# Kernel optimization log

Measured on AMD Instinct MI355X. Metric: run time of the kernel, lower is better.

## Reference

```python
import jax, jax.numpy as jnp
import numpy as np

B, I, H, M, A, R, S, O = 256, 512, 1024, 128, 2048, 4, 3, 512
RS = R * M                      # read_size = num_heads * memory_content_size
P_READ = M + S + 3              # key + shift + (beta, gate, gamma) per read head
P = R * P_READ + (3 * M + S + 3)  # write head adds erase(M) + add(M)


def setup_inputs() -> dict:
    key = jax.random.key(0)
    ks = jax.random.split(key, 16)
    x = jax.random.normal(ks[0], (B, I), dtype=jnp.float32)
    h_prev = 0.1 * jax.random.normal(ks[1], (B, H), dtype=jnp.float32)
    c_prev = 0.1 * jax.random.normal(ks[2], (B, H), dtype=jnp.float32)
    read_w_prev = jax.nn.softmax(jax.random.normal(ks[3], (B, R, A)), axis=-1)
    write_w_prev = jax.nn.softmax(jax.random.normal(ks[4], (B, A)), axis=-1)
    # init_state uses normal(mean=0.5, std=0.2) for memory
    memory_prev = 0.5 + 0.2 * jax.random.normal(ks[5], (B, M, A), dtype=jnp.float32)
    read_vec_prev = 0.1 * jax.random.normal(ks[6], (B, RS), dtype=jnp.float32)
    sc = 0.02
    Wx = sc * jax.random.normal(ks[7], (I + RS, 4 * H), dtype=jnp.float32)
    Wh = sc * jax.random.normal(ks[8], (H, 4 * H), dtype=jnp.float32)
    b_lstm = jnp.zeros((4 * H,), dtype=jnp.float32)
    Wo_h = sc * jax.random.normal(ks[9], (H, O), dtype=jnp.float32)
    bo_h = jnp.zeros((O,), dtype=jnp.float32)
    Wint = sc * jax.random.normal(ks[10], (H, P), dtype=jnp.float32)
    b_int = jnp.zeros((P,), dtype=jnp.float32)
    Wout = sc * jax.random.normal(ks[11], (RS, O), dtype=jnp.float32)
    b_out = jnp.zeros((O,), dtype=jnp.float32)
    return dict(x=x, h_prev=h_prev, c_prev=c_prev, read_w_prev=read_w_prev,
                write_w_prev=write_w_prev, memory_prev=memory_prev,
                read_vec_prev=read_vec_prev, Wx=Wx, Wh=Wh, b_lstm=b_lstm,
                Wo_h=Wo_h, bo_h=bo_h, Wint=Wint, b_int=b_int, Wout=Wout, b_out=b_out)


def _address(k, beta, g, s, gamma, w_prev, mem):
    """NTM/DNC addressing: cosine content sim -> softmax -> gate -> circular shift -> sharpen.
    k: [B,Rh,M], beta/g/gamma: [B,Rh], s: [B,Rh,S], w_prev: [B,Rh,A], mem: [B,M,A] -> w: [B,Rh,A]"""
    eps = 1e-8
    kn = jnp.linalg.norm(k, axis=-1, keepdims=True)          # [B,Rh,1]
    mn = jnp.linalg.norm(mem, axis=1)                        # [B,A]
    sim = jnp.einsum('brm,bma->bra', k, mem) / (kn * mn[:, None, :] + eps)
    w_c = jax.nn.softmax(beta[..., None] * sim, axis=-1)
    w_g = g[..., None] * w_c + (1.0 - g[..., None]) * w_prev
    # circular convolution over S shift offsets centered at 0
    rolled = jnp.stack([jnp.roll(w_g, off, axis=-1) for off in range(-(S // 2), S // 2 + 1)], axis=-1)  # [B,Rh,A,S]
    w_s = jnp.einsum('bras,brs->bra', rolled, s)
    w_pow = (w_s + 1e-12) ** gamma[..., None]
    return w_pow / (jnp.sum(w_pow, axis=-1, keepdims=True) + eps)


def reference(x, h_prev, c_prev, read_w_prev, write_w_prev, memory_prev, read_vec_prev,
              Wx, Wh, b_lstm, Wo_h, bo_h, Wint, b_int, Wout, b_out):
    b = x.shape[0]
    # ---- controller (LSTM over [input, prev read vector]) ----
    z = jnp.concatenate([x, read_vec_prev], axis=-1) @ Wx + h_prev @ Wh + b_lstm
    i_g, f_g, g_g, o_g = jnp.split(z, 4, axis=-1)
    c = jax.nn.sigmoid(f_g) * c_prev + jax.nn.sigmoid(i_g) * jnp.tanh(g_g)
    h = jax.nn.sigmoid(o_g) * jnp.tanh(c)
    output_from_hidden = h @ Wo_h + bo_h
    p = h @ Wint + b_int                                    # interface update_data
    # ---- read heads ----
    pr = p[:, :R * P_READ].reshape(b, R, P_READ)
    k_r = pr[..., :M]
    beta_r = jax.nn.softplus(pr[..., M])
    g_r = jax.nn.sigmoid(pr[..., M + 1])
    gamma_r = 1.0 + jax.nn.softplus(pr[..., M + 2])
    s_r = jax.nn.softmax(pr[..., M + 3:], axis=-1)
    w_read = _address(k_r, beta_r, g_r, s_r, gamma_r, read_w_prev, memory_prev)
    # ---- write head ----
    pw = p[:, R * P_READ:]
    k_w = pw[:, :M]
    beta_w = jax.nn.softplus(pw[:, M])
    g_w = jax.nn.sigmoid(pw[:, M + 1])
    gamma_w = 1.0 + jax.nn.softplus(pw[:, M + 2])
    s_w = jax.nn.softmax(pw[:, M + 3:M + 3 + S], axis=-1)
    erase = jax.nn.sigmoid(pw[:, M + 3 + S:2 * M + 3 + S])
    add = pw[:, 2 * M + 3 + S:]
    w_write = _address(k_w[:, None], beta_w[:, None], g_w[:, None], s_w[:, None],
                       gamma_w[:, None], write_w_prev[:, None], memory_prev)[:, 0]
    # ---- read from PREVIOUS memory (as in DNCCell.forward) ----
    read_vec = jnp.einsum('bma,bra->brm', memory_prev, w_read).reshape(b, RS)
    # ---- erase/add memory edit ----
    memory_new = memory_prev * (1.0 - jnp.einsum('bm,ba->bma', erase, w_write)) \
               + jnp.einsum('bm,ba->bma', add, w_write)
    final_output = output_from_hidden + read_vec @ Wout + b_out
    return final_output, memory_new
```

## Files before the change

### kernel.cpp

```cpp
#include <hip/hip_runtime.h>
#include <math.h>

#define B_ 256
#define I_ 512
#define H_ 1024
#define M_ 128
#define A_ 2048
#define R_ 4
#define S_ 3
#define O_ 512
#define RS_ 512
#define P_ 926
#define PW_OFF 536

typedef unsigned short ushort_t;
typedef __attribute__((ext_vector_type(8))) short bf16x8;
typedef __attribute__((ext_vector_type(4))) float f32x4;

__device__ __forceinline__ float sigmoidf_(float x) { return 1.0f / (1.0f + expf(-x)); }
__device__ __forceinline__ float softplusf_(float x) {
    return (x > 20.0f) ? x : log1pf(expf(x));
}
__device__ __forceinline__ ushort_t f2bf(float f) {
    unsigned int u = __float_as_uint(f);
    u = (u + 0x7FFFu + ((u >> 16) & 1u)) >> 16;
    return (ushort_t)u;
}

__device__ __forceinline__ float block_sum_(float v, float* red) {
    #pragma unroll
    for (int off = 32; off; off >>= 1) v += __shfl_down(v, off, 64);
    __syncthreads();
    if ((threadIdx.x & 63) == 0) red[threadIdx.x >> 6] = v;
    __syncthreads();
    return red[0] + red[1] + red[2] + red[3];
}
__device__ __forceinline__ float block_max_(float v, float* red) {
    #pragma unroll
    for (int off = 32; off; off >>= 1) v = fmaxf(v, __shfl_down(v, off, 64));
    __syncthreads();
    if ((threadIdx.x & 63) == 0) red[threadIdx.x >> 6] = v;
    __syncthreads();
    return fmaxf(fmaxf(red[0], red[1]), fmaxf(red[2], red[3]));
}

__global__ __launch_bounds__(256) void prep_kernel(
    const float* __restrict__ x, const float* __restrict__ rv,
    const float* __restrict__ hp, ushort_t* __restrict__ xin)
{
    int idx = blockIdx.x * 256 + threadIdx.x;
    int b = idx >> 11, j = idx & 2047;
    float v;
    if (j < 512)       v = x[b * 512 + j];
    else if (j < 1024) v = rv[b * 512 + (j - 512)];
    else               v = hp[b * 1024 + (j - 1024)];
    xin[idx] = f2bf(v);
}

__global__ __launch_bounds__(256) void transpose_bf16_k(
    const float* __restrict__ W, ushort_t* __restrict__ WT,
    int K, int N, int ostride, int koff)
{
    __shared__ float tile[32][33];
    int k0 = blockIdx.y * 32, n0 = blockIdx.x * 32;
    int tx = threadIdx.x & 31, ty = threadIdx.x >> 5;
    #pragma unroll
    for (int i = 0; i < 4; ++i) {
        int k = ty + i * 8;
        int n = n0 + tx;
        float v = (n < N) ? W[(size_t)(k0 + k) * N + n] : 0.0f;
        tile[tx][k] = v;
    }
    __syncthreads();
    #pragma unroll
    for (int i = 0; i < 4; ++i) {
        int nl = ty + i * 8;
        int n = n0 + nl;
        if (n < N) WT[(size_t)n * ostride + koff + k0 + tx] = f2bf(tile[nl][tx]);
    }
}

template<bool NALIGN>
__global__ __launch_bounds__(256) void gemm_bf16_k(
    const ushort_t* __restrict__ A, int lda,
    const ushort_t* __restrict__ BT, int ldb,
    const float* __restrict__ bias,
    const float* __restrict__ Cin,
    float* __restrict__ C,
    int N, int K)
{
    __shared__ ushort_t As[64][40];
    __shared__ ushort_t Bs[64][40];
    int tid = threadIdx.x;
    int bm0 = blockIdx.y * 64, bn0 = blockIdx.x * 64;
    int srow = tid >> 2;
    int scol = (tid & 3) << 3;
    int wv = tid >> 6, l = tid & 63;
    int wm = (wv & 1) * 32, wn = (wv >> 1) * 32;
    int lane16 = l & 15, quad = l >> 4;

    f32x4 z4 = {0.0f, 0.0f, 0.0f, 0.0f};
    f32x4 acc00 = z4, acc01 = z4, acc10 = z4, acc11 = z4;

    const ushort_t* ap = A + (size_t)(bm0 + srow) * lda + scol;
    bool bvalid = NALIGN || (bn0 + srow) < N;
    const ushort_t* bp = BT + (size_t)(bn0 + srow) * ldb + scol;
    float4 fz = {0.0f, 0.0f, 0.0f, 0.0f};

    for (int k0 = 0; k0 < K; k0 += 32) {
        *(float4*)&As[srow][scol] = *(const float4*)(ap + k0);
        if (bvalid) *(float4*)&Bs[srow][scol] = *(const float4*)(bp + k0);
        else        *(float4*)&Bs[srow][scol] = fz;
        __syncthreads();
        bf16x8 a0 = *(const bf16x8*)&As[wm + lane16][quad * 8];
        bf16x8 a1 = *(const bf16x8*)&As[wm + 16 + lane16][quad * 8];
        bf16x8 b0 = *(const bf16x8*)&Bs[wn + lane16][quad * 8];
        bf16x8 b1 = *(const bf16x8*)&Bs[wn + 16 + lane16][quad * 8];
        acc00 = __builtin_amdgcn_mfma_f32_16x16x32_bf16(a0, b0, acc00, 0, 0, 0);
        acc01 = __builtin_amdgcn_mfma_f32_16x16x32_bf16(a0, b1, acc01, 0, 0, 0);
        acc10 = __builtin_amdgcn_mfma_f32_16x16x32_bf16(a1, b0, acc10, 0, 0, 0);
        acc11 = __builtin_amdgcn_mfma_f32_16x16x32_bf16(a1, b1, acc11, 0, 0, 0);
        __syncthreads();
    }

    #pragma unroll
    for (int gi = 0; gi < 2; ++gi) {
        #pragma unroll
        for (int gj = 0; gj < 2; ++gj) {
            const f32x4& acc = gi == 0 ? (gj == 0 ? acc00 : acc01)
                                       : (gj == 0 ? acc10 : acc11);
            int col = bn0 + wn + gj * 16 + lane16;
            if (NALIGN || col < N) {
                float badd = bias ? bias[col] : 0.0f;
                #pragma unroll
                for (int r2 = 0; r2 < 4; ++r2) {
                    int row = bm0 + wm + gi * 16 + quad * 4 + r2;
                    float v = acc[r2] + badd;
                    if (Cin) v += Cin[(size_t)row * N + col];
                    C[(size_t)row * N + col] = v;
                }
            }
        }
    }
}

__global__ __launch_bounds__(256) void gates_kernel(
    const float* __restrict__ z, const float* __restrict__ c_prev,
    ushort_t* __restrict__ h)
{
    int idx = blockIdx.x * 256 + threadIdx.x;
    int b = idx >> 10, j = idx & 1023;
    const float* zb = z + (size_t)b * 4096;
    float zi = zb[j], zf = zb[1024 + j], zg = zb[2048 + j], zo = zb[3072 + j];
    float c = sigmoidf_(zf) * c_prev[idx] + sigmoidf_(zi) * tanhf(zg);
    h[idx] = f2bf(sigmoidf_(zo) * tanhf(c));
}

__global__ __launch_bounds__(256) void sim_kernel(
    const float* __restrict__ mem, const float* __restrict__ p,
    float* __restrict__ dots,
    float* __restrict__ mn)
{
    int b = blockIdx.y;
    int a = blockIdx.x * 256 + threadIdx.x;
    __shared__ float ks[5][M_];
    for (int idx = threadIdx.x; idx < 5 * M_; idx += 256) {
        int h = idx >> 7, m = idx & 127;
        ks[h][m] = p[(size_t)b * P_ + (h < 4 ? h * 134 + m : PW_OFF + m)];
    }
    __syncthreads();
    const float* mb = mem + (size_t)b * M_ * A_ + a;
    float d0 = 0, d1 = 0, d2 = 0, d3 = 0, d4 = 0, nn = 0;
    #pragma unroll 8
    for (int m = 0; m < M_; ++m) {
        float v = mb[(size_t)m * A_];
        d0 += v * ks[0][m]; d1 += v * ks[1][m]; d2 += v * ks[2][m];
        d3 += v * ks[3][m]; d4 += v * ks[4][m];
        nn += v * v;
    }
    size_t base = (size_t)b * 5 * A_ + a;
    dots[base + 0 * A_] = d0; dots[base + 1 * A_] = d1; dots[base + 2 * A_] = d2;
    dots[base + 3 * A_] = d3; dots[base + 4 * A_] = d4;
    mn[(size_t)b * A_ + a] = sqrtf(nn);
}

__global__ __launch_bounds__(256) void address_kernel(
    const float* __restrict__ p, const float* __restrict__ dots,
    const float* __restrict__ mn,
    const float* __restrict__ read_w_prev, const float* __restrict__ write_w_prev,
    float* __restrict__ w_read, float* __restrict__ w_write)
{
    int head = blockIdx.x;
    int b = blockIdx.y;
    int t = threadIdx.x;
    __shared__ float wg[A_];
    __shared__ float red[4];

    const float* pp = p + (size_t)b * P_ + (head < 4 ? head * 134 : PW_OFF);
    float beta  = softplusf_(pp[128]);
    float g     = sigmoidf_(pp[129]);
    float gamma = 1.0f + softplusf_(pp[130]);
    float e0 = pp[131], e1 = pp[132], e2 = pp[133];
    float smax = fmaxf(e0, fmaxf(e1, e2));
    float x0 = expf(e0 - smax), x1 = expf(e1 - smax), x2 = expf(e2 - smax);
    float sden = x0 + x1 + x2;
    float s0 = x0 / sden, s1 = x1 / sden, s2 = x2 / sden;

    float kacc = 0.0f;
    if (t < M_) { float kv = pp[t]; kacc = kv * kv; }
    float kn = sqrtf(block_sum_(kacc, red));

    const float* db = dots + ((size_t)b * 5 + head) * A_;
    const float* mb = mn + (size_t)b * A_;
    float logit[8];
    float lmax = -1e30f;
    #pragma unroll
    for (int i = 0; i < 8; ++i) {
        int a = t + 256 * i;
        float sim = db[a] / (kn * mb[a] + 1e-8f);
        logit[i] = beta * sim;
        lmax = fmaxf(lmax, logit[i]);
    }
    lmax = block_max_(lmax, red);
    float ex[8]; float lsum = 0.0f;
    #pragma unroll
    for (int i = 0; i < 8; ++i) { ex[i] = expf(logit[i] - lmax); lsum += ex[i]; }
    lsum = block_sum_(lsum, red);
    float inv_lsum = 1.0f / lsum;

    const float* wprev = (head < 4) ? read_w_prev + ((size_t)b * 4 + head) * A_
                                    : write_w_prev + (size_t)b * A_;
    #pragma unroll
    for (int i = 0; i < 8; ++i) {
        int a = t + 256 * i;
        wg[a] = g * (ex[i] * inv_lsum) + (1.0f - g) * wprev[a];
    }
    __syncthreads();
    float wpow[8]; float psum = 0.0f;
    #pragma unroll
    for (int i = 0; i < 8; ++i) {
        int a = t + 256 * i;
        float ws = s0 * wg[(a + 1) & (A_ - 1)] + s1 * wg[a] + s2 * wg[(a + A_ - 1) & (A_ - 1)];
        float wp2 = powf(ws + 1e-12f, gamma);
        wpow[i] = wp2; psum += wp2;
    }
    psum = block_sum_(psum, red);
    float inv = 1.0f / (psum + 1e-8f);
    float* wout = (head < 4) ? w_read + ((size_t)b * 4 + head) * A_
                             : w_write + (size_t)b * A_;
    #pragma unroll
    for (int i = 0; i < 8; ++i) wout[t + 256 * i] = wpow[i] * inv;
}

__global__ __launch_bounds__(256) void update_kernel(
    const float* __restrict__ mem, const float* __restrict__ p,
    const float* __restrict__ w_read, const float* __restrict__ w_write,
    float* __restrict__ mem_new,
    ushort_t* __restrict__ read_vec)
{
    int bm = blockIdx.x;
    int b = bm >> 7, m = bm & 127;
    int t = threadIdx.x;
    int wv = t >> 6, l = t & 63;
    const float* pw = p + (size_t)b * P_ + PW_OFF;
    float er = sigmoidf_(pw[134 + m]);
    float ad = pw[262 + m];
    const float* mrow = mem + ((size_t)b * M_ + m) * A_;
    const float* wwb  = w_write + (size_t)b * A_;
    const float* wr   = w_read + (size_t)b * 4 * A_;
    float* orow = mem_new + ((size_t)b * M_ + m) * A_;
    float s[4] = {0, 0, 0, 0};
    int abase = wv * 512 + l;
    #pragma unroll
    for (int i = 0; i < 8; ++i) {
        int a = abase + 64 * i;
        float v = mrow[a];
        float ww = wwb[a];
        orow[a] = v * (1.0f - er * ww) + ad * ww;
        s[0] += v * wr[a];
        s[1] += v * wr[A_ + a];
        s[2] += v * wr[2 * A_ + a];
        s[3] += v * wr[3 * A_ + a];
    }
    __shared__ float part[4][4];
    #pragma unroll
    for (int r = 0; r < 4; ++r) {
        float v = s[r];
        #pragma unroll
        for (int off = 32; off; off >>= 1) v += __shfl_down(v, off, 64);
        if (l == 0) part[wv][r] = v;
    }
    __syncthreads();
    if (t < 4) {
        float sum = part[0][t] + part[1][t] + part[2][t] + part[3][t];
        read_vec[(size_t)b * RS_ + t * M_ + m] = f2bf(sum);
    }
}

extern "C" void kernel_launch(void* const* d_in, const int* in_sizes, int n_in,
                              void* d_out, int out_size, void* d_ws, size_t ws_size,
                              hipStream_t stream) {
    const float* x            = (const float*)d_in[0];
    const float* h_prev       = (const float*)d_in[1];
    const float* c_prev       = (const float*)d_in[2];
    const float* read_w_prev  = (const float*)d_in[3];
    const float* write_w_prev = (const float*)d_in[4];
    const float* memory_prev  = (const float*)d_in[5];
    const float* read_vec_prev= (const float*)d_in[6];
    const float* Wx           = (const float*)d_in[7];
    const float* Wh           = (const float*)d_in[8];
    const float* b_lstm       = (const float*)d_in[9];
    const float* Wo_h         = (const float*)d_in[10];
    const float* bo_h         = (const float*)d_in[11];
    const float* Wint         = (const float*)d_in[12];
    const float* b_int        = (const float*)d_in[13];
    const float* Wout         = (const float*)d_in[14];
    const float* b_out        = (const float*)d_in[15];
    float* out = (float*)d_out;
    float* mem_new_out = out + (size_t)B_ * O_;

    char* wsp = (char*)d_ws;
    ushort_t* xin_bf = (ushort_t*)wsp; wsp += (size_t)B_ * 2048 * 2;
    float* z         = (float*)wsp;    wsp += (size_t)B_ * 4096 * 4;
    ushort_t* h_bf   = (ushort_t*)wsp; wsp += (size_t)B_ * H_ * 2;
    float* p         = (float*)wsp;    wsp += (size_t)B_ * P_ * 4;
    float* out_h     = (float*)wsp;    wsp += (size_t)B_ * O_ * 4;
    float* dots      = (float*)wsp;    wsp += (size_t)B_ * 5 * A_ * 4;
    float* mn        = (float*)wsp;    wsp += (size_t)B_ * A_ * 4;
    float* w_read    = (float*)wsp;    wsp += (size_t)B_ * R_ * A_ * 4;
    float* w_write   = (float*)wsp;    wsp += (size_t)B_ * A_ * 4;
    ushort_t* rv_bf  = (ushort_t*)wsp; wsp += (size_t)B_ * RS_ * 2;
    ushort_t* WxhT   = (ushort_t*)wsp; wsp += (size_t)4096 * 2048 * 2;
    ushort_t* WoT    = (ushort_t*)wsp; wsp += (size_t)512 * 1024 * 2;
    ushort_t* WintT  = (ushort_t*)wsp; wsp += (size_t)926 * 1024 * 2;
    ushort_t* WoutT  = (ushort_t*)wsp; wsp += (size_t)512 * 512 * 2;

    transpose_bf16_k<<<dim3(4096 / 32, 1024 / 32), 256, 0, stream>>>(Wx,   WxhT,  1024, 4096, 2048, 0);
    transpose_bf16_k<<<dim3(4096 / 32, 1024 / 32), 256, 0, stream>>>(Wh,   WxhT,  1024, 4096, 2048, 1024);
    transpose_bf16_k<<<dim3(512 / 32, 1024 / 32),  256, 0, stream>>>(Wo_h, WoT,   1024, 512,  1024, 0);
    transpose_bf16_k<<<dim3(29, 1024 / 32),        256, 0, stream>>>(Wint, WintT, 1024, 926,  1024, 0);
    transpose_bf16_k<<<dim3(512 / 32, 512 / 32),   256, 0, stream>>>(Wout, WoutT, 512,  512,  512,  0);

    prep_kernel<<<dim3(B_ * 2048 / 256), 256, 0, stream>>>(x, read_vec_prev, h_prev, xin_bf);
    gemm_bf16_k<true><<<dim3(4096 / 64, B_ / 64), 256, 0, stream>>>(
        xin_bf, 2048, WxhT, 2048, b_lstm, nullptr, z, 4096, 2048);
    gates_kernel<<<dim3(B_ * H_ / 256), 256, 0, stream>>>(z, c_prev, h_bf);
    gemm_bf16_k<false><<<dim3(15, B_ / 64), 256, 0, stream>>>(
        h_bf, 1024, WintT, 1024, b_int, nullptr, p, P_, 1024);
    gemm_bf16_k<true><<<dim3(O_ / 64, B_ / 64), 256, 0, stream>>>(
        h_bf, 1024, WoT, 1024, bo_h, nullptr, out_h, O_, 1024);
    sim_kernel<<<dim3(A_ / 256, B_), 256, 0, stream>>>(memory_prev, p, dots, mn);
    address_kernel<<<dim3(5, B_), 256, 0, stream>>>(
        p, dots, mn, read_w_prev, write_w_prev, w_read, w_write);
    update_kernel<<<dim3(B_ * M_), 256, 0, stream>>>(
        memory_prev, p, w_read, w_write, mem_new_out, rv_bf);
    gemm_bf16_k<true><<<dim3(O_ / 64, B_ / 64), 256, 0, stream>>>(
        rv_bf, 512, WoutT, 512, b_out, out_h, out, O_, 512);
}
```

Before: 735.4 us.

## Split-K GEMMs, merge setup kernels, concatenate projection weights, vectorize elementwise kernels

Merges the five weight-transpose launches and the input-prep launch into one setup kernel. The LSTM GEMM and the combined interface+output projection GEMM now use a 4-way split-K so small-batch GEMMs fill more CUs, and the partial sums are reduced by their consumers (gates, sim, address, update, final GEMM). The gates and update kernels use vector loads, and the address kernel switches to fast exp/log intrinsics. In exchange it writes and reads more partial-sum traffic, and every consumer re-reduces the interface partials, with slightly lower precision in the exp/pow math.

```diff
diff --git a/kernel.cpp b/kernel.cpp
--- a/kernel.cpp
+++ b/kernel.cpp
@@ -12,10 +12,13 @@
 #define RS_ 512
 #define P_ 926
 #define PW_OFF 536
+#define NP_ 1438
+#define SK_ 4
 
 typedef unsigned short ushort_t;
 typedef __attribute__((ext_vector_type(8))) short bf16x8;
 typedef __attribute__((ext_vector_type(4))) float f32x4;
+typedef __attribute__((ext_vector_type(4))) unsigned short u16x4;
 
 __device__ __forceinline__ float sigmoidf_(float x) { return 1.0f / (1.0f + expf(-x)); }
 __device__ __forceinline__ float softplusf_(float x) {
@@ -27,6 +30,14 @@
     return (ushort_t)u;
 }
 
+__device__ __forceinline__ float pval(const float* __restrict__ pp,
+                                      const float* __restrict__ b_int,
+                                      int b, int col) {
+    size_t o = (size_t)b * NP_ + col;
+    size_t st = (size_t)B_ * NP_;
+    return b_int[col] + pp[o] + pp[o + st] + pp[o + 2 * st] + pp[o + 3 * st];
+}
+
 __device__ __forceinline__ float block_sum_(float v, float* red) {
     #pragma unroll
     for (int off = 32; off; off >>= 1) v += __shfl_down(v, off, 64);
@@ -44,11 +55,50 @@
     return fmaxf(fmaxf(red[0], red[1]), fmaxf(red[2], red[3]));
 }
 
-__global__ __launch_bounds__(256) void prep_kernel(
+__device__ __forceinline__ void transpose_tile(
+    const float* __restrict__ W, ushort_t* __restrict__ WT,
+    int K, int N, int ostride, int koff, int bx, int by, float (*tile)[33])
+{
+    int k0 = by * 32, n0 = bx * 32;
+    int tx = threadIdx.x & 31, ty = threadIdx.x >> 5;
+    #pragma unroll
+    for (int i = 0; i < 4; ++i) {
+        int k = ty + i * 8;
+        int n = n0 + tx;
+        float v = (n < N) ? W[(size_t)(k0 + k) * N + n] : 0.0f;
+        tile[tx][k] = v;
+    }
+    __syncthreads();
+    #pragma unroll
+    for (int i = 0; i < 4; ++i) {
+        int nl = ty + i * 8;
+        int n = n0 + nl;
+        if (n < N) WT[(size_t)n * ostride + koff + k0 + tx] = f2bf(tile[nl][tx]);
+    }
+}
+
+__global__ __launch_bounds__(256) void setup_kernel(
     const float* __restrict__ x, const float* __restrict__ rv,
-    const float* __restrict__ hp, ushort_t* __restrict__ xin)
-{
-    int idx = blockIdx.x * 256 + threadIdx.x;
+    const float* __restrict__ hp,
+    const float* __restrict__ Wx, const float* __restrict__ Wh,
+    const float* __restrict__ Wint, const float* __restrict__ Wo_h,
+    const float* __restrict__ Wout,
+    ushort_t* __restrict__ xin, ushort_t* __restrict__ WxhT,
+    ushort_t* __restrict__ WpT, ushort_t* __restrict__ WoutT)
+{
+    __shared__ float tile[32][33];
+    int r = blockIdx.x;
+    if (r < 4096) { transpose_tile(Wx, WxhT, 1024, 4096, 2048, 0,    r % 128, r / 128, tile); return; }
+    r -= 4096;
+    if (r < 4096) { transpose_tile(Wh, WxhT, 1024, 4096, 2048, 1024, r % 128, r / 128, tile); return; }
+    r -= 4096;
+    if (r < 928)  { transpose_tile(Wint, WpT, 1024, 926, 1024, 0,    r % 29,  r / 29,  tile); return; }
+    r -= 928;
+    if (r < 512)  { transpose_tile(Wo_h, WpT + (size_t)926 * 1024, 1024, 512, 1024, 0, r % 16, r / 16, tile); return; }
+    r -= 512;
+    if (r < 256)  { transpose_tile(Wout, WoutT, 512, 512, 512, 0,    r % 16,  r / 16,  tile); return; }
+    r -= 256;
+    int idx = r * 256 + threadIdx.x;
     int b = idx >> 11, j = idx & 2047;
     float v;
     if (j < 512)       v = x[b * 512 + j];
@@ -57,42 +107,18 @@
     xin[idx] = f2bf(v);
 }
 
-__global__ __launch_bounds__(256) void transpose_bf16_k(
-    const float* __restrict__ W, ushort_t* __restrict__ WT,
-    int K, int N, int ostride, int koff)
-{
-    __shared__ float tile[32][33];
-    int k0 = blockIdx.y * 32, n0 = blockIdx.x * 32;
-    int tx = threadIdx.x & 31, ty = threadIdx.x >> 5;
-    #pragma unroll
-    for (int i = 0; i < 4; ++i) {
-        int k = ty + i * 8;
-        int n = n0 + tx;
-        float v = (n < N) ? W[(size_t)(k0 + k) * N + n] : 0.0f;
-        tile[tx][k] = v;
-    }
-    __syncthreads();
-    #pragma unroll
-    for (int i = 0; i < 4; ++i) {
-        int nl = ty + i * 8;
-        int n = n0 + nl;
-        if (n < N) WT[(size_t)n * ostride + koff + k0 + tx] = f2bf(tile[nl][tx]);
-    }
-}
-
 template<bool NALIGN>
 __global__ __launch_bounds__(256) void gemm_bf16_k(
     const ushort_t* __restrict__ A, int lda,
     const ushort_t* __restrict__ BT, int ldb,
-    const float* __restrict__ bias,
-    const float* __restrict__ Cin,
-    float* __restrict__ C,
-    int N, int K)
+    float* __restrict__ Cpart,
+    int N, int Ks)
 {
     __shared__ ushort_t As[64][40];
     __shared__ ushort_t Bs[64][40];
     int tid = threadIdx.x;
     int bm0 = blockIdx.y * 64, bn0 = blockIdx.x * 64;
+    int kbeg = blockIdx.z * Ks, kend = kbeg + Ks;
     int srow = tid >> 2;
     int scol = (tid & 3) << 3;
     int wv = tid >> 6, l = tid & 63;
@@ -107,7 +133,7 @@
     const ushort_t* bp = BT + (size_t)(bn0 + srow) * ldb + scol;
     float4 fz = {0.0f, 0.0f, 0.0f, 0.0f};
 
-    for (int k0 = 0; k0 < K; k0 += 32) {
+    for (int k0 = kbeg; k0 < kend; k0 += 32) {
         *(float4*)&As[srow][scol] = *(const float4*)(ap + k0);
         if (bvalid) *(float4*)&Bs[srow][scol] = *(const float4*)(bp + k0);
         else        *(float4*)&Bs[srow][scol] = fz;
@@ -123,6 +149,7 @@
         __syncthreads();
     }
 
+    float* C = Cpart + (size_t)blockIdx.z * gridDim.y * 64 * N;
     #pragma unroll
     for (int gi = 0; gi < 2; ++gi) {
         #pragma unroll
@@ -131,13 +158,10 @@
                                        : (gj == 0 ? acc10 : acc11);
             int col = bn0 + wn + gj * 16 + lane16;
             if (NALIGN || col < N) {
-                float badd = bias ? bias[col] : 0.0f;
                 #pragma unroll
                 for (int r2 = 0; r2 < 4; ++r2) {
                     int row = bm0 + wm + gi * 16 + quad * 4 + r2;
-                    float v = acc[r2] + badd;
-                    if (Cin) v += Cin[(size_t)row * N + col];
-                    C[(size_t)row * N + col] = v;
+                    C[(size_t)row * N + col] = acc[r2];
                 }
             }
         }
@@ -145,19 +169,37 @@
 }
 
 __global__ __launch_bounds__(256) void gates_kernel(
-    const float* __restrict__ z, const float* __restrict__ c_prev,
-    ushort_t* __restrict__ h)
-{
-    int idx = blockIdx.x * 256 + threadIdx.x;
-    int b = idx >> 10, j = idx & 1023;
-    const float* zb = z + (size_t)b * 4096;
-    float zi = zb[j], zf = zb[1024 + j], zg = zb[2048 + j], zo = zb[3072 + j];
-    float c = sigmoidf_(zf) * c_prev[idx] + sigmoidf_(zi) * tanhf(zg);
-    h[idx] = f2bf(sigmoidf_(zo) * tanhf(c));
+    const float* __restrict__ zpart, const float* __restrict__ b_lstm,
+    const float* __restrict__ c_prev, ushort_t* __restrict__ h)
+{
+    int g = blockIdx.x * 256 + threadIdx.x;
+    int b = g >> 8, j = (g & 255) << 2;
+    size_t st = (size_t)B_ * 4096;
+    size_t zb = (size_t)b * 4096 + j;
+    f32x4 zs[4];
+    #pragma unroll
+    for (int q = 0; q < 4; ++q) {
+        size_t o = zb + q * 1024;
+        f32x4 v = *(const f32x4*)(zpart + o);
+        v += *(const f32x4*)(zpart + o + st);
+        v += *(const f32x4*)(zpart + o + 2 * st);
+        v += *(const f32x4*)(zpart + o + 3 * st);
+        v += *(const f32x4*)(b_lstm + q * 1024 + j);
+        zs[q] = v;
+    }
+    f32x4 cp = *(const f32x4*)(c_prev + (size_t)b * 1024 + j);
+    u16x4 hv;
+    #pragma unroll
+    for (int e = 0; e < 4; ++e) {
+        float c = sigmoidf_(zs[1][e]) * cp[e] + sigmoidf_(zs[0][e]) * tanhf(zs[2][e]);
+        hv[e] = f2bf(sigmoidf_(zs[3][e]) * tanhf(c));
+    }
+    *(u16x4*)(h + (size_t)b * 1024 + j) = hv;
 }
 
 __global__ __launch_bounds__(256) void sim_kernel(
-    const float* __restrict__ mem, const float* __restrict__ p,
+    const float* __restrict__ mem, const float* __restrict__ pohpart,
+    const float* __restrict__ b_int,
     float* __restrict__ dots,
     float* __restrict__ mn)
 {
@@ -166,7 +208,8 @@
     __shared__ float ks[5][M_];
     for (int idx = threadIdx.x; idx < 5 * M_; idx += 256) {
         int h = idx >> 7, m = idx & 127;
-        ks[h][m] = p[(size_t)b * P_ + (h < 4 ? h * 134 + m : PW_OFF + m)];
+        int col = (h < 4) ? h * 134 + m : PW_OFF + m;
+        ks[h][m] = pval(pohpart, b_int, b, col);
     }
     __syncthreads();
     const float* mb = mem + (size_t)b * M_ * A_ + a;
@@ -185,8 +228,8 @@
 }
 
 __global__ __launch_bounds__(256) void address_kernel(
-    const float* __restrict__ p, const float* __restrict__ dots,
-    const float* __restrict__ mn,
+    const float* __restrict__ pohpart, const float* __restrict__ b_int,
+    const float* __restrict__ dots, const float* __restrict__ mn,
     const float* __restrict__ read_w_prev, const float* __restrict__ write_w_prev,
     float* __restrict__ w_read, float* __restrict__ w_write)
 {
@@ -196,18 +239,20 @@
     __shared__ float wg[A_];
     __shared__ float red[4];
 
-    const float* pp = p + (size_t)b * P_ + (head < 4 ? head * 134 : PW_OFF);
-    float beta  = softplusf_(pp[128]);
-    float g     = sigmoidf_(pp[129]);
-    float gamma = 1.0f + softplusf_(pp[130]);
-    float e0 = pp[131], e1 = pp[132], e2 = pp[133];
+    int pb = (head < 4) ? head * 134 : PW_OFF;
+    float beta  = softplusf_(pval(pohpart, b_int, b, pb + 128));
+    float g     = sigmoidf_(pval(pohpart, b_int, b, pb + 129));
+    float gamma = 1.0f + softplusf_(pval(pohpart, b_int, b, pb + 130));
+    float e0 = pval(pohpart, b_int, b, pb + 131);
+    float e1 = pval(pohpart, b_int, b, pb + 132);
+    float e2 = pval(pohpart, b_int, b, pb + 133);
     float smax = fmaxf(e0, fmaxf(e1, e2));
-    float x0 = expf(e0 - smax), x1 = expf(e1 - smax), x2 = expf(e2 - smax);
+    float x0 = __expf(e0 - smax), x1 = __expf(e1 - smax), x2 = __expf(e2 - smax);
     float sden = x0 + x1 + x2;
     float s0 = x0 / sden, s1 = x1 / sden, s2 = x2 / sden;
 
     float kacc = 0.0f;
-    if (t < M_) { float kv = pp[t]; kacc = kv * kv; }
+    if (t < M_) { float kv = pval(pohpart, b_int, b, pb + t); kacc = kv * kv; }
     float kn = sqrtf(block_sum_(kacc, red));
 
     const float* db = dots + ((size_t)b * 5 + head) * A_;
@@ -224,7 +269,7 @@
     lmax = block_max_(lmax, red);
     float ex[8]; float lsum = 0.0f;
     #pragma unroll
-    for (int i = 0; i < 8; ++i) { ex[i] = expf(logit[i] - lmax); lsum += ex[i]; }
+    for (int i = 0; i < 8; ++i) { ex[i] = __expf(logit[i] - lmax); lsum += ex[i]; }
     lsum = block_sum_(lsum, red);
     float inv_lsum = 1.0f / lsum;
 
@@ -241,7 +286,7 @@
     for (int i = 0; i < 8; ++i) {
         int a = t + 256 * i;
         float ws = s0 * wg[(a + 1) & (A_ - 1)] + s1 * wg[a] + s2 * wg[(a + A_ - 1) & (A_ - 1)];
-        float wp2 = powf(ws + 1e-12f, gamma);
+        float wp2 = __expf(gamma * __logf(ws + 1e-12f));
         wpow[i] = wp2; psum += wp2;
     }
     psum = block_sum_(psum, red);
@@ -253,7 +298,8 @@
 }
 
 __global__ __launch_bounds__(256) void update_kernel(
-    const float* __restrict__ mem, const float* __restrict__ p,
+    const float* __restrict__ mem, const float* __restrict__ pohpart,
+    const float* __restrict__ b_int,
     const float* __restrict__ w_read, const float* __restrict__ w_write,
     float* __restrict__ mem_new,
     ushort_t* __restrict__ read_vec)
@@ -262,25 +308,28 @@
     int b = bm >> 7, m = bm & 127;
     int t = threadIdx.x;
     int wv = t >> 6, l = t & 63;
-    const float* pw = p + (size_t)b * P_ + PW_OFF;
-    float er = sigmoidf_(pw[134 + m]);
-    float ad = pw[262 + m];
-    const float* mrow = mem + ((size_t)b * M_ + m) * A_;
-    const float* wwb  = w_write + (size_t)b * A_;
-    const float* wr   = w_read + (size_t)b * 4 * A_;
-    float* orow = mem_new + ((size_t)b * M_ + m) * A_;
+    float er = sigmoidf_(pval(pohpart, b_int, b, 670 + m));
+    float ad = pval(pohpart, b_int, b, 798 + m);
+    const f32x4* m4  = (const f32x4*)(mem + ((size_t)b * M_ + m) * A_);
+    const f32x4* ww4 = (const f32x4*)(w_write + (size_t)b * A_);
+    const f32x4* wr4 = (const f32x4*)(w_read + (size_t)b * 4 * A_);
+    f32x4* o4 = (f32x4*)(mem_new + ((size_t)b * M_ + m) * A_);
     float s[4] = {0, 0, 0, 0};
-    int abase = wv * 512 + l;
-    #pragma unroll
-    for (int i = 0; i < 8; ++i) {
-        int a = abase + 64 * i;
-        float v = mrow[a];
-        float ww = wwb[a];
-        orow[a] = v * (1.0f - er * ww) + ad * ww;
-        s[0] += v * wr[a];
-        s[1] += v * wr[A_ + a];
-        s[2] += v * wr[2 * A_ + a];
-        s[3] += v * wr[3 * A_ + a];
+    #pragma unroll
+    for (int j = 0; j < 2; ++j) {
+        int a4 = wv * 128 + l + 64 * j;
+        f32x4 v = m4[a4], w = ww4[a4];
+        f32x4 r0 = wr4[a4], r1 = wr4[512 + a4], r2 = wr4[1024 + a4], r3 = wr4[1536 + a4];
+        f32x4 ov;
+        #pragma unroll
+        for (int c = 0; c < 4; ++c) {
+            ov[c] = v[c] * (1.0f - er * w[c]) + ad * w[c];
+            s[0] += v[c] * r0[c];
+            s[1] += v[c] * r1[c];
+            s[2] += v[c] * r2[c];
+            s[3] += v[c] * r3[c];
+        }
+        o4[a4] = ov;
     }
     __shared__ float part[4][4];
     #pragma unroll
@@ -297,9 +346,66 @@
     }
 }
 
+__global__ __launch_bounds__(256) void gemm_final_k(
+    const ushort_t* __restrict__ A,
+    const ushort_t* __restrict__ BT,
+    const float* __restrict__ pohpart,
+    const float* __restrict__ bo_h, const float* __restrict__ b_out,
+    float* __restrict__ C)
+{
+    __shared__ ushort_t As[64][40];
+    __shared__ ushort_t Bs[64][40];
+    int tid = threadIdx.x;
+    int bm0 = blockIdx.y * 64, bn0 = blockIdx.x * 64;
+    int srow = tid >> 2, scol = (tid & 3) << 3;
+    int wv = tid >> 6, l = tid & 63;
+    int wm = (wv & 1) * 32, wn = (wv >> 1) * 32;
+    int lane16 = l & 15, quad = l >> 4;
+
+    f32x4 z4 = {0.0f, 0.0f, 0.0f, 0.0f};
+    f32x4 acc00 = z4, acc01 = z4, acc10 = z4, acc11 = z4;
+    const ushort_t* ap = A + (size_t)(bm0 + srow) * 512 + scol;
+    const ushort_t* bp = BT + (size_t)(bn0 + srow) * 512 + scol;
+
+    for (int k0 = 0; k0 < 512; k0 += 32) {
+        *(float4*)&As[srow][scol] = *(const float4*)(ap + k0);
+        *(float4*)&Bs[srow][scol] = *(const float4*)(bp + k0);
+        __syncthreads();
+        bf16x8 a0 = *(const bf16x8*)&As[wm + lane16][quad * 8];
+        bf16x8 a1 = *(const bf16x8*)&As[wm + 16 + lane16][quad * 8];
+        bf16x8 b0 = *(const bf16x8*)&Bs[wn + lane16][quad * 8];
+        bf16x8 b1 = *(const bf16x8*)&Bs[wn + 16 + lane16][quad * 8];
+        acc00 = __builtin_amdgcn_mfma_f32_16x16x32_bf16(a0, b0, acc00, 0, 0, 0);
+        acc01 = __builtin_amdgcn_mfma_f32_16x16x32_bf16(a0, b1, acc01, 0, 0, 0);
+        acc10 = __builtin_amdgcn_mfma_f32_16x16x32_bf16(a1, b0, acc10, 0, 0, 0);
+        acc11 = __builtin_amdgcn_mfma_f32_16x16x32_bf16(a1, b1, acc11, 0, 0, 0);
+        __syncthreads();
+    }
+
+    size_t st = (size_t)B_ * NP_;
+    #pragma unroll
+    for (int gi = 0; gi < 2; ++gi) {
+        #pragma unroll
+        for (int gj = 0; gj < 2; ++gj) {
+            const f32x4& acc = gi == 0 ? (gj == 0 ? acc00 : acc01)
+                                       : (gj == 0 ? acc10 : acc11);
+            int col = bn0 + wn + gj * 16 + lane16;
+            float badd = bo_h[col] + b_out[col];
+            #pragma unroll
+            for (int r2 = 0; r2 < 4; ++r2) {
+                int row = bm0 + wm + gi * 16 + quad * 4 + r2;
+                size_t o = (size_t)row * NP_ + 926 + col;
+                float oh = pohpart[o] + pohpart[o + st] + pohpart[o + 2 * st] + pohpart[o + 3 * st];
+                C[(size_t)row * 512 + col] = acc[r2] + badd + oh;
+            }
+        }
+    }
+}
+
 extern "C" void kernel_launch(void* const* d_in, const int* in_sizes, int n_in,
                               void* d_out, int out_size, void* d_ws, size_t ws_size,
                               hipStream_t stream) {
+    (void)in_sizes; (void)n_in; (void)out_size; (void)ws_size;
     const float* x            = (const float*)d_in[0];
     const float* h_prev       = (const float*)d_in[1];
     const float* c_prev       = (const float*)d_in[2];
@@ -321,39 +427,31 @@
 
     char* wsp = (char*)d_ws;
     ushort_t* xin_bf = (ushort_t*)wsp; wsp += (size_t)B_ * 2048 * 2;
-    float* z         = (float*)wsp;    wsp += (size_t)B_ * 4096 * 4;
     ushort_t* h_bf   = (ushort_t*)wsp; wsp += (size_t)B_ * H_ * 2;
-    float* p         = (float*)wsp;    wsp += (size_t)B_ * P_ * 4;
-    float* out_h     = (float*)wsp;    wsp += (size_t)B_ * O_ * 4;
+    ushort_t* rv_bf  = (ushort_t*)wsp; wsp += (size_t)B_ * RS_ * 2;
+    ushort_t* WxhT   = (ushort_t*)wsp; wsp += (size_t)4096 * 2048 * 2;
+    ushort_t* WpT    = (ushort_t*)wsp; wsp += (size_t)NP_ * 1024 * 2;
+    ushort_t* WoutT  = (ushort_t*)wsp; wsp += (size_t)512 * 512 * 2;
+    float* zpart     = (float*)wsp;    wsp += (size_t)SK_ * B_ * 4096 * 4;
+    float* pohpart   = (float*)wsp;    wsp += (size_t)SK_ * B_ * NP_ * 4;
     float* dots      = (float*)wsp;    wsp += (size_t)B_ * 5 * A_ * 4;
     float* mn        = (float*)wsp;    wsp += (size_t)B_ * A_ * 4;
     float* w_read    = (float*)wsp;    wsp += (size_t)B_ * R_ * A_ * 4;
     float* w_write   = (float*)wsp;    wsp += (size_t)B_ * A_ * 4;
-    ushort_t* rv_bf  = (ushort_t*)wsp; wsp += (size_t)B_ * RS_ * 2;
-    ushort_t* WxhT   = (ushort_t*)wsp; wsp += (size_t)4096 * 2048 * 2;
-    ushort_t* WoT    = (ushort_t*)wsp; wsp += (size_t)512 * 1024 * 2;
-    ushort_t* WintT  = (ushort_t*)wsp; wsp += (size_t)926 * 1024 * 2;
-    ushort_t* WoutT  = (ushort_t*)wsp; wsp += (size_t)512 * 512 * 2;
-
-    transpose_bf16_k<<<dim3(4096 / 32, 1024 / 32), 256, 0, stream>>>(Wx,   WxhT,  1024, 4096, 2048, 0);
-    transpose_bf16_k<<<dim3(4096 / 32, 1024 / 32), 256, 0, stream>>>(Wh,   WxhT,  1024, 4096, 2048, 1024);
-    transpose_bf16_k<<<dim3(512 / 32, 1024 / 32),  256, 0, stream>>>(Wo_h, WoT,   1024, 512,  1024, 0);
-    transpose_bf16_k<<<dim3(29, 1024 / 32),        256, 0, stream>>>(Wint, WintT, 1024, 926,  1024, 0);
-    transpose_bf16_k<<<dim3(512 / 32, 512 / 32),   256, 0, stream>>>(Wout, WoutT, 512,  512,  512,  0);
-
-    prep_kernel<<<dim3(B_ * 2048 / 256), 256, 0, stream>>>(x, read_vec_prev, h_prev, xin_bf);
-    gemm_bf16_k<true><<<dim3(4096 / 64, B_ / 64), 256, 0, stream>>>(
-        xin_bf, 2048, WxhT, 2048, b_lstm, nullptr, z, 4096, 2048);
-    gates_kernel<<<dim3(B_ * H_ / 256), 256, 0, stream>>>(z, c_prev, h_bf);
-    gemm_bf16_k<false><<<dim3(15, B_ / 64), 256, 0, stream>>>(
-        h_bf, 1024, WintT, 1024, b_int, nullptr, p, P_, 1024);
-    gemm_bf16_k<true><<<dim3(O_ / 64, B_ / 64), 256, 0, stream>>>(
-        h_bf, 1024, WoT, 1024, bo_h, nullptr, out_h, O_, 1024);
-    sim_kernel<<<dim3(A_ / 256, B_), 256, 0, stream>>>(memory_prev, p, dots, mn);
+
+    setup_kernel<<<dim3(4096 + 4096 + 928 + 512 + 256 + 2048), 256, 0, stream>>>(
+        x, read_vec_prev, h_prev, Wx, Wh, Wint, Wo_h, Wout,
+        xin_bf, WxhT, WpT, WoutT);
+    gemm_bf16_k<true><<<dim3(4096 / 64, B_ / 64, SK_), 256, 0, stream>>>(
+        xin_bf, 2048, WxhT, 2048, zpart, 4096, 2048 / SK_);
+    gates_kernel<<<dim3(B_ * H_ / 1024), 256, 0, stream>>>(zpart, b_lstm, c_prev, h_bf);
+    gemm_bf16_k<false><<<dim3(23, B_ / 64, SK_), 256, 0, stream>>>(
+        h_bf, 1024, WpT, 1024, pohpart, NP_, 1024 / SK_);
+    sim_kernel<<<dim3(A_ / 256, B_), 256, 0, stream>>>(memory_prev, pohpart, b_int, dots, mn);
     address_kernel<<<dim3(5, B_), 256, 0, stream>>>(
-        p, dots, mn, read_w_prev, write_w_prev, w_read, w_write);
+        pohpart, b_int, dots, mn, read_w_prev, write_w_prev, w_read, w_write);
     update_kernel<<<dim3(B_ * M_), 256, 0, stream>>>(
-        memory_prev, p, w_read, w_write, mem_new_out, rv_bf);
-    gemm_bf16_k<true><<<dim3(O_ / 64, B_ / 64), 256, 0, stream>>>(
-        rv_bf, 512, WoutT, 512, b_out, out_h, out, O_, 512);
-}
+        memory_prev, pohpart, b_int, w_read, w_write, mem_new_out, rv_bf);
+    gemm_final_k<<<dim3(O_ / 64, B_ / 64), 256, 0, stream>>>(
+        rv_bf, WoutT, pohpart, bo_h, b_out, out);
+}
```

Result: faster. 670.9 us (-8.8%).
